# Performance work log

Measured on AMD Instinct MI355X. Metric: run time of the kernel, lower is better.

The kernel has to match this reference:

```python
import jax, jax.numpy as jnp
import numpy as np

B, Z, A = 1024, 512, 8          # batch_size, z_dim, action_dim
AH, ZH = 64, 512                # action_hidden_dim, z_hidden_dim
N_NEG = 100                     # n_neg_actions
TEMP = 0.1                      # temperature
TOP_K = (1, 3, 10)


def forward_model(z, a, Wa, ba, W1, b1, W2, b2):
    # MLP forward model with skip connection (z_delta=True):
    # embed action, concat with z, 2-layer MLP predicting a delta.
    h_a = jax.nn.relu(a @ Wa + ba)                                   # [..., AH]
    h = jax.nn.relu(jnp.concatenate([jnp.broadcast_to(z, a.shape[:-1] + (Z,)), h_a], axis=-1) @ W1 + b1)  # [..., ZH]
    delta = h @ W2 + b2                                              # [..., Z]
    return z + delta


def setup_inputs() -> dict:
    key = jax.random.key(0)
    ks = jax.random.split(key, 8)
    def w(k, shape, fan_in):
        return jax.random.normal(k, shape, jnp.float32) / np.float32(np.sqrt(fan_in))
    z = jax.random.normal(ks[0], (B, Z), jnp.float32)
    z_next = jax.random.normal(ks[1], (B, Z), jnp.float32)
    z_next_hat = jax.random.normal(ks[2], (B, Z), jnp.float32)
    actions = jax.random.normal(ks[3], (B, A), jnp.float32)
    Wa = w(ks[4], (A, AH), A)
    ba = jnp.zeros((AH,), jnp.float32)
    W1 = w(ks[5], (Z + AH, ZH), Z + AH)
    b1 = jnp.zeros((ZH,), jnp.float32)
    W2 = w(ks[6], (ZH, Z), ZH)
    b2 = jnp.zeros((Z,), jnp.float32)
    return {"z": z, "z_next": z_next, "z_next_hat": z_next_hat, "actions": actions,
            "Wa": Wa, "ba": ba, "W1": W1, "b1": b1, "W2": W2, "b2": b2}


def reference(z, z_next, z_next_hat, actions, Wa, ba, W1, b1, W2, b2):
    # ControlCPC.compute_loss with dot_product_similarity, vectorized:
    # the Python loop over n_neg_actions rolled-action forward-model calls
    # becomes one batched [n-1, B, ...] forward-model evaluation.
    batch = z.shape[0]
    n = min(N_NEG, batch)
    sim = z_next @ z_next_hat.T                                      # [B, B] positives on diagonal
    shifts = jnp.arange(1, n)
    neg_actions = jax.vmap(lambda i: jnp.roll(actions, -i, axis=0))(shifts)  # [n-1, B, A]
    z_hat_neg = forward_model(z[None], neg_actions, Wa, ba, W1, b1, W2, b2)  # [n-1, B, Z]
    neg_sim = jnp.einsum('nbz,bz->bn', z_hat_neg, z_next)            # diag of similarity per shift
    sim_mat = jnp.concatenate([sim, neg_sim], axis=1)                # [B, B+n-1]
    # INCE loss, positives on diagonal
    logp = jax.nn.log_softmax(sim_mat / jnp.float32(TEMP), axis=1)
    loss = -jnp.mean(jnp.diagonal(logp))                             # diagonal takes first B entries
    labels = jnp.arange(batch)[:, None]
    accs = []
    for k in TOP_K:
        _, preds = jax.lax.top_k(sim_mat, k)                         # [B, k]
        accs.append(jnp.mean((preds == labels).astype(jnp.float32)) * k)
    return (loss, accs[0], accs[1], accs[2])
```

## Files before the change

kernel.cpp:

```cpp
#include <hip/hip_runtime.h>
#include <math.h>

#define B_SZ 1024
#define Z_DIM 512
#define A_DIM 8
#define AH 64
#define ZH 512
#define NNEG 99
#define ROWLEN (B_SZ + NNEG)
#define INV_T 10.0f

__global__ __launch_bounds__(256) void fused_gemm(
    const float* __restrict__ z, const float* __restrict__ z_next,
    const float* __restrict__ z_next_hat, const float* __restrict__ actions,
    const float* __restrict__ Wa, const float* __restrict__ ba,
    const float* __restrict__ W1, const float* __restrict__ b1,
    const float* __restrict__ W2,
    float* __restrict__ sim, float* __restrict__ u, float* __restrict__ v,
    float* __restrict__ g)
{
    constexpr int BK = 32;
    __shared__ float As[BK][68];
    __shared__ float Bs[BK][68];
    __shared__ float sact[64][A_DIM];
    __shared__ float sWa[A_DIM * AH];
    __shared__ float sba[AH];

    const int id = blockIdx.x;
    const int tid = threadIdx.x;

    const float* A; const float* Bm; const float* bias = nullptr;
    float* C; int N, K; bool transb; int seg; int bm0, bn0;
    if (id < 256) {
        seg = 0; int t = id; bn0 = (t & 15) * 64; bm0 = (t >> 4) * 64;
        A = z_next; Bm = z_next_hat; C = sim; N = 1024; K = 512; transb = true;
    } else if (id < 384) {
        seg = 1; int t = id - 256; bn0 = (t & 7) * 64; bm0 = (t >> 3) * 64;
        A = z; Bm = W1; C = u; N = 512; K = 512; transb = false; bias = b1;
    } else if (id < 512) {
        seg = 2; int t = id - 384; bn0 = (t & 7) * 64; bm0 = (t >> 3) * 64;
        A = z_next; Bm = W2; C = v; N = 512; K = 512; transb = true;
    } else {
        seg = 3; int t = id - 512; bn0 = (t & 7) * 64; bm0 = (t >> 3) * 64;
        A = nullptr; Bm = W1 + Z_DIM * ZH; C = g; N = 512; K = 64; transb = false;
    }

    if (seg == 3) {
        for (int i = tid; i < 64 * A_DIM; i += 256)
            (&sact[0][0])[i] = actions[bm0 * A_DIM + i];
        for (int i = tid; i < A_DIM * AH; i += 256) sWa[i] = Wa[i];
        if (tid < AH) sba[tid] = ba[tid];
    }
    __syncthreads();

    const int tm = (tid >> 4) << 2;
    const int tn = (tid & 15) << 2;
    float acc[4][4] = {};

    for (int k0 = 0; k0 < K; k0 += BK) {
        if (seg == 3) {
#pragma unroll
            for (int i = 0; i < 8; ++i) {
                int lin = tid + i * 256;
                int c = lin & 31, r = lin >> 5;
                int kc = k0 + c;
                float val = sba[kc];
#pragma unroll
                for (int k = 0; k < A_DIM; ++k) val += sact[r][k] * sWa[k * AH + kc];
                As[c][r] = fmaxf(val, 0.0f);
            }
        } else {
#pragma unroll
            for (int i = 0; i < 2; ++i) {
                int f = tid + i * 256;
                int r = f >> 3, c = (f & 7) * 4;
                float4 av = *(const float4*)&A[(bm0 + r) * K + k0 + c];
                As[c + 0][r] = av.x; As[c + 1][r] = av.y;
                As[c + 2][r] = av.z; As[c + 3][r] = av.w;
            }
        }
        if (transb) {
#pragma unroll
            for (int i = 0; i < 2; ++i) {
                int f = tid + i * 256;
                int r = f >> 3, c = (f & 7) * 4;
                float4 bv = *(const float4*)&Bm[(bn0 + r) * K + k0 + c];
                Bs[c + 0][r] = bv.x; Bs[c + 1][r] = bv.y;
                Bs[c + 2][r] = bv.z; Bs[c + 3][r] = bv.w;
            }
        } else {
#pragma unroll
            for (int i = 0; i < 2; ++i) {
                int f = tid + i * 256;
                int r = f >> 4, c = (f & 15) * 4;
                *(float4*)&Bs[r][c] = *(const float4*)&Bm[(k0 + r) * N + bn0 + c];
            }
        }
        __syncthreads();
#pragma unroll
        for (int k = 0; k < BK; ++k) {
            float4 a4 = *(const float4*)&As[k][tm];
            float4 b4 = *(const float4*)&Bs[k][tn];
            float a[4] = {a4.x, a4.y, a4.z, a4.w};
            float b[4] = {b4.x, b4.y, b4.z, b4.w};
#pragma unroll
            for (int i = 0; i < 4; ++i)
#pragma unroll
                for (int j = 0; j < 4; ++j) acc[i][j] += a[i] * b[j];
        }
        __syncthreads();
    }
#pragma unroll
    for (int i = 0; i < 4; ++i) {
        int r = bm0 + tm + i;
        float4 o = {acc[i][0], acc[i][1], acc[i][2], acc[i][3]};
        if (bias) {
            o.x += bias[bn0 + tn + 0]; o.y += bias[bn0 + tn + 1];
            o.z += bias[bn0 + tn + 2]; o.w += bias[bn0 + tn + 3];
        }
        *(float4*)&C[r * N + bn0 + tn] = o;
    }
}

__global__ __launch_bounds__(256) void row_kernel(const float* __restrict__ sim,
                                                  const float* __restrict__ u,
                                                  const float* __restrict__ v,
                                                  const float* __restrict__ g,
                                                  const float* __restrict__ z,
                                                  const float* __restrict__ z_next,
                                                  const float* __restrict__ b2,
                                                  float* __restrict__ acc) {
    int b = blockIdx.x;
    int tid = threadIdx.x;
    int wave = tid >> 6, lane = tid & 63;
    __shared__ float su[ZH];
    __shared__ float sv[ZH];
    __shared__ float row[ROWLEN];
    __shared__ float redc0[4], redmax[4], redes[4];
    __shared__ int redcnt[4];

    {
        const float4* u4 = (const float4*)(u + b * ZH);
        const float4* v4 = (const float4*)(v + b * ZH);
        if (tid < ZH / 4) {
            *(float4*)&su[tid * 4] = u4[tid];
            *(float4*)&sv[tid * 4] = v4[tid];
        }
        const float4* s4 = (const float4*)(sim + b * B_SZ);
        *(float4*)&row[tid * 4] = s4[tid];
    }
    float p = 0.0f;
    {
        const float4* z4 = (const float4*)(z + b * Z_DIM);
        const float4* zn4 = (const float4*)(z_next + b * Z_DIM);
        const float4* b24 = (const float4*)b2;
        if (tid < Z_DIM / 4) {
            float4 a = z4[tid], c = b24[tid], n = zn4[tid];
            p = (a.x + c.x) * n.x + (a.y + c.y) * n.y + (a.z + c.z) * n.z + (a.w + c.w) * n.w;
        }
    }
    for (int off = 32; off; off >>= 1) p += __shfl_down(p, off);
    if (lane == 0) redc0[wave] = p;
    __syncthreads();

    float c0 = redc0[0] + redc0[1] + redc0[2] + redc0[3];

    for (int s = 1 + wave; s <= NNEG; s += 4) {
        int jr = (b + s) & (B_SZ - 1);
        const float4* gr4 = (const float4*)(g + jr * ZH);
        float d = 0.0f;
#pragma unroll
        for (int i = 0; i < 2; ++i) {
            int t4 = lane + i * 64;
            float4 gv = gr4[t4];
            float4 uv = *(const float4*)&su[t4 * 4];
            float4 vv = *(const float4*)&sv[t4 * 4];
            d += fmaxf(uv.x + gv.x, 0.0f) * vv.x;
            d += fmaxf(uv.y + gv.y, 0.0f) * vv.y;
            d += fmaxf(uv.z + gv.z, 0.0f) * vv.z;
            d += fmaxf(uv.w + gv.w, 0.0f) * vv.w;
        }
        for (int off = 32; off; off >>= 1) d += __shfl_down(d, off);
        if (lane == 0) row[B_SZ + s - 1] = c0 + d;
    }
    __syncthreads();

    float diag = row[b];
    float m = -3.4e38f;
    for (int j = tid; j < ROWLEN; j += 256) m = fmaxf(m, row[j]);
    for (int off = 32; off; off >>= 1) m = fmaxf(m, __shfl_down(m, off));
    if (lane == 0) redmax[wave] = m;
    __syncthreads();
    m = fmaxf(fmaxf(redmax[0], redmax[1]), fmaxf(redmax[2], redmax[3]));

    float es = 0.0f;
    int cnt = 0;
    for (int j = tid; j < ROWLEN; j += 256) {
        float x = row[j];
        es += __expf((x - m) * INV_T);
        if (x > diag) cnt++;
        else if (j < b && x == diag) cnt++;
    }
    for (int off = 32; off; off >>= 1) {
        es += __shfl_down(es, off);
        cnt += __shfl_down(cnt, off);
    }
    __syncthreads();
    if (lane == 0) { redes[wave] = es; redcnt[wave] = cnt; }
    __syncthreads();
    if (tid == 0) {
        float esum = redes[0] + redes[1] + redes[2] + redes[3];
        int rank = redcnt[0] + redcnt[1] + redcnt[2] + redcnt[3];
        float loss_b = (m - diag) * INV_T + logf(esum);
        atomicAdd(&acc[0], loss_b);
        if (rank < 1) atomicAdd(&acc[1], 1.0f);
        if (rank < 3) atomicAdd(&acc[2], 1.0f);
        if (rank < 10) atomicAdd(&acc[3], 1.0f);
    }
}

__global__ void finalize_kernel(const float* __restrict__ acc, float* __restrict__ out) {
    int t = threadIdx.x;
    if (t < 4) out[t] = acc[t] * (1.0f / (float)B_SZ);
}

extern "C" void kernel_launch(void* const* d_in, const int* in_sizes, int n_in,
                              void* d_out, int out_size, void* d_ws, size_t ws_size,
                              hipStream_t stream) {
    const float* z          = (const float*)d_in[0];
    const float* z_next     = (const float*)d_in[1];
    const float* z_next_hat = (const float*)d_in[2];
    const float* actions    = (const float*)d_in[3];
    const float* Wa         = (const float*)d_in[4];
    const float* ba         = (const float*)d_in[5];
    const float* W1         = (const float*)d_in[6];
    const float* b1         = (const float*)d_in[7];
    const float* W2         = (const float*)d_in[8];
    const float* b2         = (const float*)d_in[9];
    float* out = (float*)d_out;

    float* ws  = (float*)d_ws;
    float* sim = ws;
    float* u   = sim + B_SZ * B_SZ;
    float* v   = u + B_SZ * ZH;
    float* g   = v + B_SZ * ZH;
    float* acc = g + B_SZ * ZH;

    hipMemsetAsync(acc, 0, 4 * sizeof(float), stream);

    fused_gemm<<<640, 256, 0, stream>>>(z, z_next, z_next_hat, actions, Wa, ba,
                                        W1, b1, W2, sim, u, v, g);
    row_kernel<<<B_SZ, 256, 0, stream>>>(sim, u, v, g, z, z_next, b2, acc);
    finalize_kernel<<<1, 64, 0, stream>>>(acc, out);
}
```

Measured before the change: 141.0 us.

## Use split-bf16 MFMA for the large GEMMs and fold finalize into the row kernel

The three K=512 GEMM segments move from scalar FP32 FMA tiles to MFMA bf16 16x16x32 instructions. Each operand is split into hi and lo bf16 parts and three products are accumulated to keep close to FP32 accuracy. The separate memset and finalize kernel are replaced by per-row partial results plus a last-block-done counter that does the final reduction inside row_kernel. This cuts two launches and uses the matrix cores, at the cost of conversion work, a slightly different numerical error profile, and a fence/atomic completion pattern.

Measured after the change: 134.0 us. -5.0%, faster.

```diff
diff --git a/kernel.cpp b/kernel.cpp
--- a/kernel.cpp
+++ b/kernel.cpp
@@ -10,6 +10,21 @@
 #define ROWLEN (B_SZ + NNEG)
 #define INV_T 10.0f
 
+typedef __attribute__((ext_vector_type(8))) short short8;
+typedef __attribute__((ext_vector_type(4))) float f32x4;
+
+__device__ __forceinline__ void cvt_hilo(float4 x0, float4 x1, short8& hi, short8& lo) {
+    float xs[8] = {x0.x, x0.y, x0.z, x0.w, x1.x, x1.y, x1.z, x1.w};
+#pragma unroll
+    for (int i = 0; i < 8; ++i) {
+        unsigned u = __float_as_uint(xs[i]);
+        hi[i] = (short)(u >> 16);
+        float hf = __uint_as_float(u & 0xffff0000u);
+        float lf = xs[i] - hf;
+        lo[i] = (short)(__float_as_uint(lf) >> 16);
+    }
+}
+
 __global__ __launch_bounds__(256) void fused_gemm(
     const float* __restrict__ z, const float* __restrict__ z_next,
     const float* __restrict__ z_next_hat, const float* __restrict__ actions,
@@ -17,48 +32,30 @@
     const float* __restrict__ W1, const float* __restrict__ b1,
     const float* __restrict__ W2,
     float* __restrict__ sim, float* __restrict__ u, float* __restrict__ v,
-    float* __restrict__ g)
+    float* __restrict__ g, unsigned* __restrict__ cnt)
 {
-    constexpr int BK = 32;
-    __shared__ float As[BK][68];
-    __shared__ float Bs[BK][68];
+    __shared__ float LA[64][68];
+    __shared__ float LB[64][68];
     __shared__ float sact[64][A_DIM];
     __shared__ float sWa[A_DIM * AH];
     __shared__ float sba[AH];
 
     const int id = blockIdx.x;
     const int tid = threadIdx.x;
-
-    const float* A; const float* Bm; const float* bias = nullptr;
-    float* C; int N, K; bool transb; int seg; int bm0, bn0;
-    if (id < 256) {
-        seg = 0; int t = id; bn0 = (t & 15) * 64; bm0 = (t >> 4) * 64;
-        A = z_next; Bm = z_next_hat; C = sim; N = 1024; K = 512; transb = true;
-    } else if (id < 384) {
-        seg = 1; int t = id - 256; bn0 = (t & 7) * 64; bm0 = (t >> 3) * 64;
-        A = z; Bm = W1; C = u; N = 512; K = 512; transb = false; bias = b1;
-    } else if (id < 512) {
-        seg = 2; int t = id - 384; bn0 = (t & 7) * 64; bm0 = (t >> 3) * 64;
-        A = z_next; Bm = W2; C = v; N = 512; K = 512; transb = true;
-    } else {
-        seg = 3; int t = id - 512; bn0 = (t & 7) * 64; bm0 = (t >> 3) * 64;
-        A = nullptr; Bm = W1 + Z_DIM * ZH; C = g; N = 512; K = 64; transb = false;
-    }
-
-    if (seg == 3) {
+    if (id == 0 && tid == 0) *cnt = 0;
+
+    if (id >= 512) {
+        int t = id - 512;
+        int bn0 = (t & 7) * 64, bm0 = (t >> 3) * 64;
+        const float* W1h = W1 + Z_DIM * ZH;
         for (int i = tid; i < 64 * A_DIM; i += 256)
             (&sact[0][0])[i] = actions[bm0 * A_DIM + i];
         for (int i = tid; i < A_DIM * AH; i += 256) sWa[i] = Wa[i];
         if (tid < AH) sba[tid] = ba[tid];
-    }
-    __syncthreads();
-
-    const int tm = (tid >> 4) << 2;
-    const int tn = (tid & 15) << 2;
-    float acc[4][4] = {};
-
-    for (int k0 = 0; k0 < K; k0 += BK) {
-        if (seg == 3) {
+        __syncthreads();
+        int tm = (tid >> 4) << 2, tn = (tid & 15) << 2;
+        float acc[4][4] = {};
+        for (int k0 = 0; k0 < 64; k0 += 32) {
 #pragma unroll
             for (int i = 0; i < 8; ++i) {
                 int lin = tid + i * 256;
@@ -67,59 +64,115 @@
                 float val = sba[kc];
 #pragma unroll
                 for (int k = 0; k < A_DIM; ++k) val += sact[r][k] * sWa[k * AH + kc];
-                As[c][r] = fmaxf(val, 0.0f);
-            }
-        } else {
-#pragma unroll
-            for (int i = 0; i < 2; ++i) {
-                int f = tid + i * 256;
-                int r = f >> 3, c = (f & 7) * 4;
-                float4 av = *(const float4*)&A[(bm0 + r) * K + k0 + c];
-                As[c + 0][r] = av.x; As[c + 1][r] = av.y;
-                As[c + 2][r] = av.z; As[c + 3][r] = av.w;
-            }
-        }
-        if (transb) {
-#pragma unroll
-            for (int i = 0; i < 2; ++i) {
-                int f = tid + i * 256;
-                int r = f >> 3, c = (f & 7) * 4;
-                float4 bv = *(const float4*)&Bm[(bn0 + r) * K + k0 + c];
-                Bs[c + 0][r] = bv.x; Bs[c + 1][r] = bv.y;
-                Bs[c + 2][r] = bv.z; Bs[c + 3][r] = bv.w;
-            }
-        } else {
+                LA[c][r] = fmaxf(val, 0.0f);
+            }
 #pragma unroll
             for (int i = 0; i < 2; ++i) {
                 int f = tid + i * 256;
                 int r = f >> 4, c = (f & 15) * 4;
-                *(float4*)&Bs[r][c] = *(const float4*)&Bm[(k0 + r) * N + bn0 + c];
+                *(float4*)&LB[r][c] = *(const float4*)&W1h[(k0 + r) * ZH + bn0 + c];
+            }
+            __syncthreads();
+#pragma unroll
+            for (int k = 0; k < 32; ++k) {
+                float4 a4 = *(const float4*)&LA[k][tm];
+                float4 b4 = *(const float4*)&LB[k][tn];
+                float a[4] = {a4.x, a4.y, a4.z, a4.w};
+                float b[4] = {b4.x, b4.y, b4.z, b4.w};
+#pragma unroll
+                for (int i = 0; i < 4; ++i)
+#pragma unroll
+                    for (int j = 0; j < 4; ++j) acc[i][j] += a[i] * b[j];
+            }
+            __syncthreads();
+        }
+#pragma unroll
+        for (int i = 0; i < 4; ++i) {
+            float4 o = {acc[i][0], acc[i][1], acc[i][2], acc[i][3]};
+            *(float4*)&g[(bm0 + tm + i) * ZH + bn0 + tn] = o;
+        }
+        return;
+    }
+
+    const float* Aop; const float* Bop; const float* bias = nullptr;
+    float* C; int N; bool btrans; int bm0, bn0;
+    if (id < 256) {
+        int t = id; bn0 = (t & 15) * 64; bm0 = (t >> 4) * 64;
+        Aop = z_next; Bop = z_next_hat; C = sim; N = 1024; btrans = true;
+    } else if (id < 384) {
+        int t = id - 256; bn0 = (t & 7) * 64; bm0 = (t >> 3) * 64;
+        Aop = z; Bop = W1; C = u; N = 512; btrans = false; bias = b1;
+    } else {
+        int t = id - 384; bn0 = (t & 7) * 64; bm0 = (t >> 3) * 64;
+        Aop = z_next; Bop = W2; C = v; N = 512; btrans = true;
+    }
+
+    const int lane = tid & 63, wv = tid >> 6;
+    const int lm = lane & 15, lq = lane >> 4;
+    const int wm = (wv >> 1) * 32, wn = (wv & 1) * 32;
+    f32x4 acc[2][2] = {};
+
+    for (int k0 = 0; k0 < 512; k0 += 64) {
+#pragma unroll
+        for (int i = 0; i < 4; ++i) {
+            int gg = tid + i * 256;
+            int r = gg >> 4, c4 = (gg & 15) << 2;
+            *(float4*)&LA[r][c4] = *(const float4*)&Aop[(bm0 + r) * 512 + k0 + c4];
+        }
+        if (btrans) {
+#pragma unroll
+            for (int i = 0; i < 4; ++i) {
+                int gg = tid + i * 256;
+                int r = gg >> 4, c4 = (gg & 15) << 2;
+                *(float4*)&LB[r][c4] = *(const float4*)&Bop[(bn0 + r) * 512 + k0 + c4];
+            }
+        } else {
+#pragma unroll
+            for (int i = 0; i < 4; ++i) {
+                int gg = tid + i * 256;
+                int kr = gg >> 4, n4 = (gg & 15) << 2;
+                float4 w = *(const float4*)&Bop[(k0 + kr) * 512 + bn0 + n4];
+                LB[n4 + 0][kr] = w.x; LB[n4 + 1][kr] = w.y;
+                LB[n4 + 2][kr] = w.z; LB[n4 + 3][kr] = w.w;
             }
         }
         __syncthreads();
 #pragma unroll
-        for (int k = 0; k < BK; ++k) {
-            float4 a4 = *(const float4*)&As[k][tm];
-            float4 b4 = *(const float4*)&Bs[k][tn];
-            float a[4] = {a4.x, a4.y, a4.z, a4.w};
-            float b[4] = {b4.x, b4.y, b4.z, b4.w};
-#pragma unroll
-            for (int i = 0; i < 4; ++i)
-#pragma unroll
-                for (int j = 0; j < 4; ++j) acc[i][j] += a[i] * b[j];
+        for (int kk = 0; kk < 64; kk += 32) {
+            int kb = kk + lq * 8;
+            short8 ah[2], al[2], bh[2], bl[2];
+#pragma unroll
+            for (int i = 0; i < 2; ++i) {
+                float4 x0 = *(const float4*)&LA[wm + i * 16 + lm][kb];
+                float4 x1 = *(const float4*)&LA[wm + i * 16 + lm][kb + 4];
+                cvt_hilo(x0, x1, ah[i], al[i]);
+                float4 y0 = *(const float4*)&LB[wn + i * 16 + lm][kb];
+                float4 y1 = *(const float4*)&LB[wn + i * 16 + lm][kb + 4];
+                cvt_hilo(y0, y1, bh[i], bl[i]);
+            }
+#pragma unroll
+            for (int i = 0; i < 2; ++i)
+#pragma unroll
+                for (int j = 0; j < 2; ++j) {
+                    acc[i][j] = __builtin_amdgcn_mfma_f32_16x16x32_bf16(ah[i], bh[j], acc[i][j], 0, 0, 0);
+                    acc[i][j] = __builtin_amdgcn_mfma_f32_16x16x32_bf16(ah[i], bl[j], acc[i][j], 0, 0, 0);
+                    acc[i][j] = __builtin_amdgcn_mfma_f32_16x16x32_bf16(al[i], bh[j], acc[i][j], 0, 0, 0);
+                }
         }
         __syncthreads();
     }
 #pragma unroll
-    for (int i = 0; i < 4; ++i) {
-        int r = bm0 + tm + i;
-        float4 o = {acc[i][0], acc[i][1], acc[i][2], acc[i][3]};
-        if (bias) {
-            o.x += bias[bn0 + tn + 0]; o.y += bias[bn0 + tn + 1];
-            o.z += bias[bn0 + tn + 2]; o.w += bias[bn0 + tn + 3];
-        }
-        *(float4*)&C[r * N + bn0 + tn] = o;
-    }
+    for (int i = 0; i < 2; ++i)
+#pragma unroll
+        for (int j = 0; j < 2; ++j) {
+            int n = bn0 + wn + j * 16 + lm;
+            float bb = bias ? bias[n] : 0.0f;
+#pragma unroll
+            for (int r = 0; r < 4; ++r) {
+                int m = bm0 + wm + i * 16 + lq * 4 + r;
+                C[m * N + n] = acc[i][j][r] + bb;
+            }
+        }
 }
 
 __global__ __launch_bounds__(256) void row_kernel(const float* __restrict__ sim,
@@ -129,7 +182,9 @@
                                                   const float* __restrict__ z,
                                                   const float* __restrict__ z_next,
                                                   const float* __restrict__ b2,
-                                                  float* __restrict__ acc) {
+                                                  float* __restrict__ pw,
+                                                  unsigned* __restrict__ cnt,
+                                                  float* __restrict__ out) {
     int b = blockIdx.x;
     int tid = threadIdx.x;
     int wave = tid >> 6, lane = tid & 63;
@@ -138,6 +193,8 @@
     __shared__ float row[ROWLEN];
     __shared__ float redc0[4], redmax[4], redes[4];
     __shared__ int redcnt[4];
+    __shared__ float red[256];
+    __shared__ int sdone;
 
     {
         const float4* u4 = (const float4*)(u + b * ZH);
@@ -194,34 +251,46 @@
     m = fmaxf(fmaxf(redmax[0], redmax[1]), fmaxf(redmax[2], redmax[3]));
 
     float es = 0.0f;
-    int cnt = 0;
+    int cntk = 0;
     for (int j = tid; j < ROWLEN; j += 256) {
         float x = row[j];
         es += __expf((x - m) * INV_T);
-        if (x > diag) cnt++;
-        else if (j < b && x == diag) cnt++;
+        if (x > diag) cntk++;
+        else if (j < b && x == diag) cntk++;
     }
     for (int off = 32; off; off >>= 1) {
         es += __shfl_down(es, off);
-        cnt += __shfl_down(cnt, off);
-    }
-    __syncthreads();
-    if (lane == 0) { redes[wave] = es; redcnt[wave] = cnt; }
+        cntk += __shfl_down(cntk, off);
+    }
+    __syncthreads();
+    if (lane == 0) { redes[wave] = es; redcnt[wave] = cntk; }
     __syncthreads();
     if (tid == 0) {
         float esum = redes[0] + redes[1] + redes[2] + redes[3];
         int rank = redcnt[0] + redcnt[1] + redcnt[2] + redcnt[3];
         float loss_b = (m - diag) * INV_T + logf(esum);
-        atomicAdd(&acc[0], loss_b);
-        if (rank < 1) atomicAdd(&acc[1], 1.0f);
-        if (rank < 3) atomicAdd(&acc[2], 1.0f);
-        if (rank < 10) atomicAdd(&acc[3], 1.0f);
-    }
-}
-
-__global__ void finalize_kernel(const float* __restrict__ acc, float* __restrict__ out) {
-    int t = threadIdx.x;
-    if (t < 4) out[t] = acc[t] * (1.0f / (float)B_SZ);
+        pw[b * 4 + 0] = loss_b;
+        pw[b * 4 + 1] = (rank < 1) ? 1.0f : 0.0f;
+        pw[b * 4 + 2] = (rank < 3) ? 1.0f : 0.0f;
+        pw[b * 4 + 3] = (rank < 10) ? 1.0f : 0.0f;
+        __threadfence();
+        unsigned old = atomicAdd(cnt, 1u);
+        sdone = (old == B_SZ - 1) ? 1 : 0;
+    }
+    __syncthreads();
+    if (sdone) {
+        __threadfence();
+        int c = tid & 3;
+        float s = 0.0f;
+        for (int r = tid >> 2; r < B_SZ; r += 64) s += pw[r * 4 + c];
+        red[tid] = s;
+        __syncthreads();
+        if (tid < 4) {
+            float t = 0.0f;
+            for (int gg = 0; gg < 64; ++gg) t += red[tid + gg * 4];
+            out[tid] = t * (1.0f / (float)B_SZ);
+        }
+    }
 }
 
 extern "C" void kernel_launch(void* const* d_in, const int* in_sizes, int n_in,
@@ -244,12 +313,10 @@
     float* u   = sim + B_SZ * B_SZ;
     float* v   = u + B_SZ * ZH;
     float* g   = v + B_SZ * ZH;
-    float* acc = g + B_SZ * ZH;
-
-    hipMemsetAsync(acc, 0, 4 * sizeof(float), stream);
+    float* pw  = g + B_SZ * ZH;
+    unsigned* cnt = (unsigned*)(pw + B_SZ * 4);
 
     fused_gemm<<<640, 256, 0, stream>>>(z, z_next, z_next_hat, actions, Wa, ba,
-                                        W1, b1, W2, sim, u, v, g);
-    row_kernel<<<B_SZ, 256, 0, stream>>>(sim, u, v, g, z, z_next, b2, acc);
-    finalize_kernel<<<1, 64, 0, stream>>>(acc, out);
+                                        W1, b1, W2, sim, u, v, g, cnt);
+    row_kernel<<<B_SZ, 256, 0, stream>>>(sim, u, v, g, z, z_next, b2, pw, cnt, out);
 }
```
